# Kernel tuning notes

Measured on AMD Instinct MI355X. Metric: run time of the kernel, lower is better.

The kernel has to match this reference:

```python
import jax, jax.numpy as jnp
import numpy as np

N_NODES = 100000
N_FEAT = 512
HIDDEN = 64
N_CLASS = 40
N_EDGES = 3200000


def setup_inputs() -> dict:
    key = jax.random.key(0)
    k1, k2, k3, k4, k5, k6 = jax.random.split(key, 6)
    x = jax.random.normal(k1, (N_NODES, N_FEAT), dtype=jnp.float32)
    edge_index = jax.random.randint(k2, (2, N_EDGES), 0, N_NODES, dtype=jnp.int64)
    # Glorot-style init like PyG GCNConv
    s1 = (6.0 / (N_FEAT + HIDDEN)) ** 0.5
    s2 = (6.0 / (HIDDEN + N_CLASS)) ** 0.5
    W1 = jax.random.uniform(k3, (N_FEAT, HIDDEN), jnp.float32, -s1, s1)
    b1 = jnp.zeros((HIDDEN,), jnp.float32)
    W2 = jax.random.uniform(k4, (HIDDEN, N_CLASS), jnp.float32, -s2, s2)
    b2 = jnp.zeros((N_CLASS,), jnp.float32)
    return {"x": x, "edge_index": edge_index, "W1": W1, "b1": b1, "W2": W2, "b2": b2}


def _gcn_norm(edge_index, n_nodes):
    # add self-loops, symmetric normalization (PyG gcn_norm defaults)
    loops = jnp.arange(n_nodes, dtype=edge_index.dtype)
    src = jnp.concatenate([edge_index[0], loops])
    dst = jnp.concatenate([edge_index[1], loops])
    deg = jax.ops.segment_sum(jnp.ones_like(dst, dtype=jnp.float32), dst,
                              num_segments=n_nodes)
    dinv = jnp.where(deg > 0, jax.lax.rsqrt(deg), 0.0)
    norm = dinv[src] * dinv[dst]  # [E + N]
    return src, dst, norm


def _gcn_conv(h, src, dst, norm, W, b, n_nodes):
    h = h @ W                                   # [N, out]
    msg = h[src] * norm[:, None]                # gather + scale, [E+N, out]
    out = jax.ops.segment_sum(msg, dst, num_segments=n_nodes)  # scatter-add
    return out + b


def reference(x, edge_index, W1, b1, W2, b2):
    n = x.shape[0]
    src, dst, norm = _gcn_norm(edge_index, n)
    h = _gcn_conv(x, src, dst, norm, W1, b1, n)
    h = jax.nn.relu(h)
    h = _gcn_conv(h, src, dst, norm, W2, b2, n)
    return jax.nn.softmax(h, axis=-1)
```

## Files before the change

kernel.cpp:

```cpp
#include <hip/hip_runtime.h>
#include <hip/hip_bf16.h>
#include <math.h>

#define NFEAT 512
#define HID   64
#define NCLS  40
#define T2STRIDE 64

#define BSHIFT 9
#define BSIZE  512
#define BCAP   20480
#define CHUNK  4096

typedef __attribute__((ext_vector_type(8))) short bf16x8v;
typedef __attribute__((ext_vector_type(4))) float f32x4v;

__device__ __forceinline__ float rl_f(float v, int l) {
    return __int_as_float(__builtin_amdgcn_readlane(__float_as_int(v), l));
}
__device__ __forceinline__ unsigned short f2bf(float f) {
    __hip_bfloat16 h = __float2bfloat16(f);
    return *(unsigned short*)&h;
}


__global__ __launch_bounds__(256) void bin_scatter(const int* __restrict__ ei, int e,
                                                   int nbuckets,
                                                   int* __restrict__ bucket_cursor,
                                                   int* __restrict__ stage) {
    __shared__ int packed_s[CHUNK];
    __shared__ unsigned char bkt_s[CHUNK];
    __shared__ int hist[256];
    __shared__ int base_s[256];
    __shared__ int lcur[256];
    int t = threadIdx.x;
    int b0 = blockIdx.x * CHUNK;
    int cnt = min(CHUNK, e - b0);
    for (int i = t; i < 256; i += 256) hist[i] = 0;
    __syncthreads();
    for (int i = t; i < cnt; i += 256) {
        int s = ei[b0 + i];
        int d = ei[e + b0 + i];
        packed_s[i] = (s << BSHIFT) | (d & (BSIZE - 1));
        bkt_s[i] = (unsigned char)(d >> BSHIFT);
        atomicAdd(&hist[d >> BSHIFT], 1);
    }
    __syncthreads();
    for (int i = t; i < nbuckets; i += 256) {
        int c = hist[i];
        base_s[i] = c ? atomicAdd(&bucket_cursor[i], c) : 0;
        lcur[i] = 0;
    }
    __syncthreads();
    for (int i = t; i < cnt; i += 256) {
        int bk = bkt_s[i];
        int pos = base_s[bk] + atomicAdd(&lcur[bk], 1);
        if (pos < BCAP) stage[(size_t)bk * BCAP + pos] = packed_s[i];
    }
}

__global__ __launch_bounds__(256) void bucket_csr(const int* __restrict__ stage,
                                                  const int* __restrict__ bucket_cursor,
                                                  int* __restrict__ row_ptr,
                                                  float* __restrict__ dinv,
                                                  int* __restrict__ col,
                                                  int n, int e, int nbuckets) {
    __shared__ int sc[256];
    __shared__ int hist[BSIZE];
    __shared__ int lbase[BSIZE];
    __shared__ int psum[256];
    int b = blockIdx.x;
    int t = threadIdx.x;
    int v = (t < nbuckets) ? bucket_cursor[t] : 0;
    sc[t] = v;
    __syncthreads();
    #pragma unroll
    for (int off = 1; off < 256; off <<= 1) {
        int u = (t >= off) ? sc[t - off] : 0;
        __syncthreads();
        sc[t] += u;
        __syncthreads();
    }
    int base0 = (b > 0) ? sc[b - 1] : 0;
    if (b == 0 && t == 0) row_ptr[n] = e;

    int cnt = min(bucket_cursor[b], BCAP);
    int node0 = b << BSHIFT;
    int nnodes = min(BSIZE, n - node0);
    const int* st = stage + (size_t)b * BCAP;
    for (int i = t; i < BSIZE; i += 256) hist[i] = 0;
    __syncthreads();
    for (int i = t; i < cnt; i += 256) atomicAdd(&hist[st[i] & (BSIZE - 1)], 1);
    __syncthreads();
    int h0 = hist[2 * t], h1 = hist[2 * t + 1];
    int pair = h0 + h1;
    psum[t] = pair;
    __syncthreads();
    #pragma unroll
    for (int off = 1; off < 256; off <<= 1) {
        int u = (t >= off) ? psum[t - off] : 0;
        __syncthreads();
        psum[t] += u;
        __syncthreads();
    }
    int ex = psum[t] - pair;
    lbase[2 * t] = ex;
    lbase[2 * t + 1] = ex + h0;
    __syncthreads();
    for (int i = t; i < nnodes; i += 256) {
        row_ptr[node0 + i] = base0 + lbase[i];
        dinv[node0 + i] = rsqrtf((float)(hist[i] + 1));
    }
    __syncthreads();
    for (int i = t; i < cnt; i += 256) {
        int p = st[i];
        int pos = atomicAdd(&lbase[p & (BSIZE - 1)], 1);
        col[base0 + pos] = ((unsigned)p) >> BSHIFT;
    }
}


__global__ __launch_bounds__(256) void w1_to_bf16t(const float* __restrict__ W1,
                                                   unsigned short* __restrict__ w1bt) {
    int idx = blockIdx.x * 256 + threadIdx.x;
    int c = idx >> 9, k = idx & 511;
    w1bt[idx] = f2bf(W1[k * HID + c]);
}


__global__ __launch_bounds__(256) void gemm1(const float* __restrict__ x,
                                             const unsigned short* __restrict__ w1bt,
                                             const float* __restrict__ dinv,
                                             __hip_bfloat16* __restrict__ t1, int n) {
    __shared__ __align__(16) unsigned short As[64][40];
    __shared__ __align__(16) unsigned short Bs[64][40];
    int t = threadIdx.x;
    int m0 = blockIdx.x * 64;
    int w = t >> 6, lane = t & 63;
    int lrow = lane & 15, lkg = lane >> 4;
    f32x4v acc[4] = {};

    int arow = t >> 2;
    int akg = t & 3;
    int grow = m0 + arow; if (grow >= n) grow = n - 1;
    const float* xrow = x + (size_t)grow * NFEAT;

    for (int k0 = 0; k0 < NFEAT; k0 += 32) {
        float4 v0 = *(const float4*)(xrow + k0 + akg * 8);
        float4 v1 = *(const float4*)(xrow + k0 + akg * 8 + 4);
        union { unsigned short u[8]; uint4 q; } P;
        P.u[0] = f2bf(v0.x); P.u[1] = f2bf(v0.y); P.u[2] = f2bf(v0.z); P.u[3] = f2bf(v0.w);
        P.u[4] = f2bf(v1.x); P.u[5] = f2bf(v1.y); P.u[6] = f2bf(v1.z); P.u[7] = f2bf(v1.w);
        *(uint4*)&As[arow][akg * 8] = P.q;
        *(uint4*)&Bs[arow][akg * 8] = *(const uint4*)(w1bt + arow * 512 + k0 + akg * 8);
        __syncthreads();
        bf16x8v af = *(const bf16x8v*)&As[w * 16 + lrow][lkg * 8];
        #pragma unroll
        for (int nb = 0; nb < 4; nb++) {
            bf16x8v bfv = *(const bf16x8v*)&Bs[nb * 16 + lrow][lkg * 8];
            acc[nb] = __builtin_amdgcn_mfma_f32_16x16x32_bf16(af, bfv, acc[nb], 0, 0, 0);
        }
        __syncthreads();
    }
    #pragma unroll
    for (int r = 0; r < 4; r++) {
        int row = m0 + w * 16 + lkg * 4 + r;
        if (row < n) {
            float d = dinv[row];
            #pragma unroll
            for (int nb = 0; nb < 4; nb++) {
                t1[(size_t)row * HID + nb * 16 + lrow] = __float2bfloat16(acc[nb][r] * d);
            }
        }
    }
}


#define UNPACK_ADD(pv) do { \
    acc[0] += __uint_as_float((pv).x << 16); acc[1] += __uint_as_float((pv).x & 0xffff0000u); \
    acc[2] += __uint_as_float((pv).y << 16); acc[3] += __uint_as_float((pv).y & 0xffff0000u); \
    acc[4] += __uint_as_float((pv).z << 16); acc[5] += __uint_as_float((pv).z & 0xffff0000u); \
    acc[6] += __uint_as_float((pv).w << 16); acc[7] += __uint_as_float((pv).w & 0xffff0000u); } while (0)

__global__ __launch_bounds__(256) void agg1_gemm2(const __hip_bfloat16* __restrict__ t1,
                                                  const int* __restrict__ row_ptr,
                                                  const int* __restrict__ col,
                                                  const float* __restrict__ dinv,
                                                  const float* __restrict__ b1,
                                                  const float* __restrict__ W2,
                                                  __hip_bfloat16* __restrict__ t2, int n) {
    __shared__ float2 w2p[32 * 40];
    for (int i = threadIdx.x; i < 32 * 40; i += 256) {
        int k2 = i / 40, c = i - k2 * 40;
        w2p[i] = make_float2(W2[(2 * k2) * 40 + c], W2[(2 * k2 + 1) * 40 + c]);
    }
    __syncthreads();

    int wave = threadIdx.x >> 6;
    int lane = threadIdx.x & 63;
    int node0 = blockIdx.x * 4 + wave;
    int node = (node0 < n) ? node0 : n - 1;
    int r = lane & 7;
    int slot = lane >> 3;

    const uint4* t1q = (const uint4*)t1;
    int s0 = row_ptr[node], s1 = row_ptr[node + 1];

    float acc[8] = {0.f, 0.f, 0.f, 0.f, 0.f, 0.f, 0.f, 0.f};

    if (lane < 8) {
        uint4 pv = t1q[(size_t)node * 8 + lane];
        UNPACK_ADD(pv);
    }

    int bpbase = slot * 4;
    for (int jb = s0; jb < s1; jb += 32) {
        int rem = s1 - jb;
        int ll = lane & 31;
        int cidx = col[jb + ((ll < rem) ? ll : 0)];
        int srcg[4];
        #pragma unroll
        for (int g = 0; g < 4; g++) {
            int src = __builtin_amdgcn_ds_bpermute(bpbase + 32 * g, cidx);
            srcg[g] = (8 * g + slot < rem) ? src : n;
        }
        uint4 pv[4];
        #pragma unroll
        for (int g = 0; g < 4; g++) pv[g] = t1q[(size_t)srcg[g] * 8 + r];
        #pragma unroll
        for (int g = 0; g < 4; g++) { UNPACK_ADD(pv[g]); }
    }

    #pragma unroll
    for (int off = 8; off < 64; off <<= 1) {
        #pragma unroll
        for (int j = 0; j < 8; j++) acc[j] += __shfl_xor(acc[j], off, 64);
    }

    float dn = dinv[node];
    const float4* b1q = (const float4*)b1;
    float4 ba = b1q[2 * r];
    float4 bb = b1q[2 * r + 1];
    float hv[8];
    hv[0] = fmaxf(0.f, dn * acc[0] + ba.x);
    hv[1] = fmaxf(0.f, dn * acc[1] + ba.y);
    hv[2] = fmaxf(0.f, dn * acc[2] + ba.z);
    hv[3] = fmaxf(0.f, dn * acc[3] + ba.w);
    hv[4] = fmaxf(0.f, dn * acc[4] + bb.x);
    hv[5] = fmaxf(0.f, dn * acc[5] + bb.y);
    hv[6] = fmaxf(0.f, dn * acc[6] + bb.z);
    hv[7] = fmaxf(0.f, dn * acc[7] + bb.w);

    int c = (lane < 40) ? lane : 39;
    float o = 0.0f;
    #pragma unroll
    for (int rr = 0; rr < 8; rr++) {
        #pragma unroll
        for (int j2 = 0; j2 < 4; j2++) {
            float ha = rl_f(hv[2 * j2],     rr);
            float hb = rl_f(hv[2 * j2 + 1], rr);
            float2 wv = w2p[(4 * rr + j2) * 40 + c];
            o += ha * wv.x + hb * wv.y;
        }
    }
    if (node0 < n && lane < 40)
        t2[(size_t)node * T2STRIDE + lane] = __float2bfloat16(dn * o);
}


__global__ __launch_bounds__(256) void agg2_softmax(const __hip_bfloat16* __restrict__ t2,
                                                    const int* __restrict__ row_ptr,
                                                    const int* __restrict__ col,
                                                    const float* __restrict__ dinv,
                                                    const float* __restrict__ b2,
                                                    float* __restrict__ out, int n) {
    int wave = threadIdx.x >> 6;
    int lane = threadIdx.x & 63;
    int node = blockIdx.x * 4 + wave;
    if (node >= n) return;
    int h = lane >> 5;
    int p = lane & 31;
    int pc = (p < 20) ? p : 19;
    const unsigned* t2d = (const unsigned*)t2;
    int s0 = row_ptr[node], s1 = row_ptr[node + 1];

    float ax = 0.f, ay = 0.f;
    if (h == 0) {
        unsigned v = t2d[(size_t)node * 32 + pc];
        ax = __uint_as_float(v << 16);
        ay = __uint_as_float(v & 0xffff0000u);
    }
    for (int jb = s0; jb < s1; jb += 16) {
        int rem = s1 - jb;
        int cv = col[jb + ((lane < rem) ? lane : 0)];
        int srcg[8];
        #pragma unroll
        for (int i = 0; i < 8; i++) {
            int eid = 2 * i + h;
            int src = __builtin_amdgcn_ds_bpermute(4 * eid, cv);
            srcg[i] = (eid < rem) ? src : n;
        }
        unsigned pv[8];
        #pragma unroll
        for (int i = 0; i < 8; i++) pv[i] = t2d[(size_t)srcg[i] * 32 + pc];
        #pragma unroll
        for (int i = 0; i < 8; i++) {
            ax += __uint_as_float(pv[i] << 16);
            ay += __uint_as_float(pv[i] & 0xffff0000u);
        }
    }
    ax += __shfl_xor(ax, 32, 64);
    ay += __shfl_xor(ay, 32, 64);

    float dn = dinv[node];
    float2 bv = *(const float2*)(b2 + 2 * pc);
    float lx = dn * ax + bv.x;
    float ly = dn * ay + bv.y;
    float m = (p < 20) ? fmaxf(lx, ly) : -INFINITY;
    #pragma unroll
    for (int off = 16; off; off >>= 1) m = fmaxf(m, __shfl_xor(m, off, 64));
    float ex = (p < 20) ? expf(lx - m) : 0.0f;
    float ey = (p < 20) ? expf(ly - m) : 0.0f;
    float ssum = ex + ey;
    #pragma unroll
    for (int off = 16; off; off >>= 1) ssum += __shfl_xor(ssum, off, 64);
    if (h == 0 && p < 20) {
        *(float2*)(out + (size_t)node * NCLS + 2 * p) = make_float2(ex / ssum, ey / ssum);
    }
}


static inline size_t align256(size_t x) { return (x + 255) & ~(size_t)255; }

extern "C" void kernel_launch(void* const* d_in, const int* in_sizes, int n_in,
                              void* d_out, int out_size, void* d_ws, size_t ws_size,
                              hipStream_t stream) {
    const float* x  = (const float*)d_in[0];
    const int*   ei = (const int*)d_in[1];
    const float* W1 = (const float*)d_in[2];
    const float* b1 = (const float*)d_in[3];
    const float* W2 = (const float*)d_in[4];
    const float* b2 = (const float*)d_in[5];
    float* out = (float*)d_out;

    const int n = in_sizes[0] / NFEAT;
    const int e = in_sizes[1] / 2;
    const int nbuckets = (n + BSIZE - 1) >> BSHIFT;

    char* ws = (char*)d_ws;
    size_t off = 0;
    int*   row_ptr  = (int*)(ws + off);   off += align256((size_t)(n + 1) * 4);
    float* dinv     = (float*)(ws + off); off += align256((size_t)n * 4);
    int*   bcursor  = (int*)(ws + off);   off += align256(256 * 4);
    int*   col      = (int*)(ws + off);   off += align256((size_t)e * 4);
    int*   stage    = (int*)(ws + off);   off += align256((size_t)nbuckets * BCAP * 4);
    unsigned short* w1bt = (unsigned short*)(ws + off); off += align256((size_t)HID * NFEAT * 2);
    __hip_bfloat16* t1 = (__hip_bfloat16*)(ws + off); off += align256((size_t)(n + 1) * HID * 2);
    __hip_bfloat16* t2 = (__hip_bfloat16*)(ws + off); off += align256((size_t)(n + 1) * T2STRIDE * 2);

    (void)hipMemsetAsync(bcursor, 0, 256 * 4, stream);
    (void)hipMemsetAsync(t1 + (size_t)n * HID, 0, HID * 2, stream);
    (void)hipMemsetAsync(t2 + (size_t)n * T2STRIDE, 0, T2STRIDE * 2, stream);
    w1_to_bf16t<<<(HID * NFEAT) / 256, 256, 0, stream>>>(W1, w1bt);
    bin_scatter<<<(e + CHUNK - 1) / CHUNK, 256, 0, stream>>>(ei, e, nbuckets, bcursor, stage);
    bucket_csr<<<nbuckets, 256, 0, stream>>>(stage, bcursor, row_ptr, dinv, col, n, e, nbuckets);
    gemm1<<<(n + 63) / 64, 256, 0, stream>>>(x, w1bt, dinv, t1, n);
    agg1_gemm2<<<(n + 3) / 4, 256, 0, stream>>>(t1, row_ptr, col, dinv, b1, W2, t2, n);
    agg2_softmax<<<(n + 3) / 4, 256, 0, stream>>>(t2, row_ptr, col, dinv, b2, out, n);
}
```

Baseline: 550.8 us.

## Chunk features into 16-column slabs and reorder layer-2 aggregate before GEMM

Stores t1 and the hidden activations as four column-chunked slabs (32 bytes per node) so each aggregation block gathers from a smaller, more cache-resident table. A generic agg_pass kernel is launched twice. Each launch has blocks interleaved across chunks and halves of the node range, and each wave handles several nodes. Layer 2 now aggregates the 64-wide hidden features first and applies W2 afterwards in finish2, which adds fp32 intermediate round trips, extra launches, and 64- instead of 40-wide gathers for the second layer.

```diff
diff --git a/kernel.cpp b/kernel.cpp
--- a/kernel.cpp
+++ b/kernel.cpp
@@ -5,7 +5,7 @@
 #define NFEAT 512
 #define HID   64
 #define NCLS  40
-#define T2STRIDE 64
+#define NPW   4
 
 #define BSHIFT 9
 #define BSIZE  512
@@ -121,17 +121,21 @@
 
 
 __global__ __launch_bounds__(256) void w1_to_bf16t(const float* __restrict__ W1,
-                                                   unsigned short* __restrict__ w1bt) {
+                                                   unsigned short* __restrict__ w1bt,
+                                                   unsigned short* __restrict__ t1c, int n) {
     int idx = blockIdx.x * 256 + threadIdx.x;
     int c = idx >> 9, k = idx & 511;
     w1bt[idx] = f2bf(W1[k * HID + c]);
+    if (blockIdx.x == 0 && threadIdx.x < 32) {
+        ((unsigned*)t1c)[((size_t)(threadIdx.x >> 3) * (n + 1) + n) * 8 + (threadIdx.x & 7)] = 0;
+    }
 }
 
 
 __global__ __launch_bounds__(256) void gemm1(const float* __restrict__ x,
                                              const unsigned short* __restrict__ w1bt,
                                              const float* __restrict__ dinv,
-                                             __hip_bfloat16* __restrict__ t1, int n) {
+                                             unsigned short* __restrict__ t1c, int n) {
     __shared__ __align__(16) unsigned short As[64][40];
     __shared__ __align__(16) unsigned short Bs[64][40];
     int t = threadIdx.x;
@@ -169,164 +173,131 @@
             float d = dinv[row];
             #pragma unroll
             for (int nb = 0; nb < 4; nb++) {
-                t1[(size_t)row * HID + nb * 16 + lrow] = __float2bfloat16(acc[nb][r] * d);
+                t1c[((size_t)nb * (n + 1) + row) * 16 + lrow] =
+                    f2bf(acc[nb][r] * d);
             }
         }
     }
 }
 
 
-#define UNPACK_ADD(pv) do { \
-    acc[0] += __uint_as_float((pv).x << 16); acc[1] += __uint_as_float((pv).x & 0xffff0000u); \
-    acc[2] += __uint_as_float((pv).y << 16); acc[3] += __uint_as_float((pv).y & 0xffff0000u); \
-    acc[4] += __uint_as_float((pv).z << 16); acc[5] += __uint_as_float((pv).z & 0xffff0000u); \
-    acc[6] += __uint_as_float((pv).w << 16); acc[7] += __uint_as_float((pv).w & 0xffff0000u); } while (0)
-
-__global__ __launch_bounds__(256) void agg1_gemm2(const __hip_bfloat16* __restrict__ t1,
-                                                  const int* __restrict__ row_ptr,
-                                                  const int* __restrict__ col,
-                                                  const float* __restrict__ dinv,
-                                                  const float* __restrict__ b1,
-                                                  const float* __restrict__ W2,
-                                                  __hip_bfloat16* __restrict__ t2, int n) {
+__global__ __launch_bounds__(256) void agg_pass(const unsigned short* __restrict__ tc,
+                                                const int* __restrict__ row_ptr,
+                                                const int* __restrict__ col,
+                                                float* __restrict__ aggOut,
+                                                int n, int nsplit) {
+    int bid = blockIdx.x;
+    int x = bid & 7;
+    int chunk = x >> 1;
+    int half = x & 1;
+    int g = bid >> 3;
+    int wave = threadIdx.x >> 6;
+    int lane = threadIdx.x & 63;
+    int f = lane & 7;
+    int slot = lane >> 3;
+    const unsigned* tcu = (const unsigned*)tc + (size_t)chunk * (n + 1) * 8;
+    int nodebase = g * (4 * NPW) + wave * NPW + half * nsplit;
+    int nend = half ? n : nsplit;
+
+    for (int ni = 0; ni < NPW; ni++) {
+        int node = nodebase + ni;
+        if (node >= nend) break;
+        int s0 = row_ptr[node], s1 = row_ptr[node + 1];
+        float a0 = 0.f, a1 = 0.f;
+        if (slot == 0) {
+            unsigned v = tcu[node * 8 + f];
+            a0 = __uint_as_float(v << 16);
+            a1 = __uint_as_float(v & 0xffff0000u);
+        }
+        for (int jb = s0; jb < s1; jb += 64) {
+            int rem = s1 - jb;
+            int cv = col[jb + ((lane < rem) ? lane : 0)];
+            int src[8];
+            #pragma unroll
+            for (int i = 0; i < 8; i++) {
+                int eid = 8 * i + slot;
+                int sv = __builtin_amdgcn_ds_bpermute(4 * eid, cv);
+                src[i] = (eid < rem) ? sv : n;
+            }
+            unsigned pv[8];
+            #pragma unroll
+            for (int i = 0; i < 8; i++) pv[i] = tcu[src[i] * 8 + f];
+            #pragma unroll
+            for (int i = 0; i < 8; i++) {
+                a0 += __uint_as_float(pv[i] << 16);
+                a1 += __uint_as_float(pv[i] & 0xffff0000u);
+            }
+        }
+        #pragma unroll
+        for (int off = 8; off < 64; off <<= 1) {
+            a0 += __shfl_xor(a0, off, 64);
+            a1 += __shfl_xor(a1, off, 64);
+        }
+        if (slot == 0) {
+            *(float2*)(aggOut + (size_t)node * HID + chunk * 16 + 2 * f) =
+                make_float2(a0, a1);
+        }
+    }
+}
+
+
+__global__ __launch_bounds__(256) void finish1(const float* __restrict__ aggA,
+                                               const float* __restrict__ dinv,
+                                               const float* __restrict__ b1,
+                                               unsigned short* __restrict__ gc, int n) {
+    int t = threadIdx.x;
+    unsigned* gcu = (unsigned*)gc;
+    if (blockIdx.x == 0 && t < 32) {
+        gcu[((size_t)(t >> 3) * (n + 1) + n) * 8 + (t & 7)] = 0;
+    }
+    int idx = blockIdx.x * 256 + t;
+    int node = idx >> 5;
+    int fp = idx & 31;
+    if (node >= n) return;
+    float2 a = *(const float2*)(aggA + (size_t)node * HID + 2 * fp);
+    float dn = dinv[node];
+    float2 bv = *(const float2*)(b1 + 2 * fp);
+    float g0 = dn * fmaxf(0.f, dn * a.x + bv.x);
+    float g1 = dn * fmaxf(0.f, dn * a.y + bv.y);
+    unsigned p = ((unsigned)f2bf(g1) << 16) | (unsigned)f2bf(g0);
+    gcu[((size_t)(fp >> 3) * (n + 1) + node) * 8 + (fp & 7)] = p;
+}
+
+
+__global__ __launch_bounds__(256) void finish2(const float* __restrict__ aggB,
+                                               const float* __restrict__ dinv,
+                                               const float* __restrict__ W2,
+                                               const float* __restrict__ b2,
+                                               float* __restrict__ out, int n) {
     __shared__ float2 w2p[32 * 40];
     for (int i = threadIdx.x; i < 32 * 40; i += 256) {
         int k2 = i / 40, c = i - k2 * 40;
-        w2p[i] = make_float2(W2[(2 * k2) * 40 + c], W2[(2 * k2 + 1) * 40 + c]);
-    }
-    __syncthreads();
-
-    int wave = threadIdx.x >> 6;
-    int lane = threadIdx.x & 63;
-    int node0 = blockIdx.x * 4 + wave;
-    int node = (node0 < n) ? node0 : n - 1;
-    int r = lane & 7;
-    int slot = lane >> 3;
-
-    const uint4* t1q = (const uint4*)t1;
-    int s0 = row_ptr[node], s1 = row_ptr[node + 1];
-
-    float acc[8] = {0.f, 0.f, 0.f, 0.f, 0.f, 0.f, 0.f, 0.f};
-
-    if (lane < 8) {
-        uint4 pv = t1q[(size_t)node * 8 + lane];
-        UNPACK_ADD(pv);
-    }
-
-    int bpbase = slot * 4;
-    for (int jb = s0; jb < s1; jb += 32) {
-        int rem = s1 - jb;
-        int ll = lane & 31;
-        int cidx = col[jb + ((ll < rem) ? ll : 0)];
-        int srcg[4];
-        #pragma unroll
-        for (int g = 0; g < 4; g++) {
-            int src = __builtin_amdgcn_ds_bpermute(bpbase + 32 * g, cidx);
-            srcg[g] = (8 * g + slot < rem) ? src : n;
-        }
-        uint4 pv[4];
-        #pragma unroll
-        for (int g = 0; g < 4; g++) pv[g] = t1q[(size_t)srcg[g] * 8 + r];
-        #pragma unroll
-        for (int g = 0; g < 4; g++) { UNPACK_ADD(pv[g]); }
-    }
-
-    #pragma unroll
-    for (int off = 8; off < 64; off <<= 1) {
-        #pragma unroll
-        for (int j = 0; j < 8; j++) acc[j] += __shfl_xor(acc[j], off, 64);
-    }
-
-    float dn = dinv[node];
-    const float4* b1q = (const float4*)b1;
-    float4 ba = b1q[2 * r];
-    float4 bb = b1q[2 * r + 1];
-    float hv[8];
-    hv[0] = fmaxf(0.f, dn * acc[0] + ba.x);
-    hv[1] = fmaxf(0.f, dn * acc[1] + ba.y);
-    hv[2] = fmaxf(0.f, dn * acc[2] + ba.z);
-    hv[3] = fmaxf(0.f, dn * acc[3] + ba.w);
-    hv[4] = fmaxf(0.f, dn * acc[4] + bb.x);
-    hv[5] = fmaxf(0.f, dn * acc[5] + bb.y);
-    hv[6] = fmaxf(0.f, dn * acc[6] + bb.z);
-    hv[7] = fmaxf(0.f, dn * acc[7] + bb.w);
-
-    int c = (lane < 40) ? lane : 39;
-    float o = 0.0f;
-    #pragma unroll
-    for (int rr = 0; rr < 8; rr++) {
-        #pragma unroll
-        for (int j2 = 0; j2 < 4; j2++) {
-            float ha = rl_f(hv[2 * j2],     rr);
-            float hb = rl_f(hv[2 * j2 + 1], rr);
-            float2 wv = w2p[(4 * rr + j2) * 40 + c];
-            o += ha * wv.x + hb * wv.y;
-        }
-    }
-    if (node0 < n && lane < 40)
-        t2[(size_t)node * T2STRIDE + lane] = __float2bfloat16(dn * o);
-}
-
-
-__global__ __launch_bounds__(256) void agg2_softmax(const __hip_bfloat16* __restrict__ t2,
-                                                    const int* __restrict__ row_ptr,
-                                                    const int* __restrict__ col,
-                                                    const float* __restrict__ dinv,
-                                                    const float* __restrict__ b2,
-                                                    float* __restrict__ out, int n) {
-    int wave = threadIdx.x >> 6;
-    int lane = threadIdx.x & 63;
+        w2p[i] = make_float2(W2[(2 * k2) * NCLS + c], W2[(2 * k2 + 1) * NCLS + c]);
+    }
+    __syncthreads();
+    int wave = threadIdx.x >> 6, lane = threadIdx.x & 63;
     int node = blockIdx.x * 4 + wave;
     if (node >= n) return;
-    int h = lane >> 5;
-    int p = lane & 31;
-    int pc = (p < 20) ? p : 19;
-    const unsigned* t2d = (const unsigned*)t2;
-    int s0 = row_ptr[node], s1 = row_ptr[node + 1];
-
-    float ax = 0.f, ay = 0.f;
-    if (h == 0) {
-        unsigned v = t2d[(size_t)node * 32 + pc];
-        ax = __uint_as_float(v << 16);
-        ay = __uint_as_float(v & 0xffff0000u);
-    }
-    for (int jb = s0; jb < s1; jb += 16) {
-        int rem = s1 - jb;
-        int cv = col[jb + ((lane < rem) ? lane : 0)];
-        int srcg[8];
-        #pragma unroll
-        for (int i = 0; i < 8; i++) {
-            int eid = 2 * i + h;
-            int src = __builtin_amdgcn_ds_bpermute(4 * eid, cv);
-            srcg[i] = (eid < rem) ? src : n;
-        }
-        unsigned pv[8];
-        #pragma unroll
-        for (int i = 0; i < 8; i++) pv[i] = t2d[(size_t)srcg[i] * 32 + pc];
-        #pragma unroll
-        for (int i = 0; i < 8; i++) {
-            ax += __uint_as_float(pv[i] << 16);
-            ay += __uint_as_float(pv[i] & 0xffff0000u);
-        }
-    }
-    ax += __shfl_xor(ax, 32, 64);
-    ay += __shfl_xor(ay, 32, 64);
-
-    float dn = dinv[node];
-    float2 bv = *(const float2*)(b2 + 2 * pc);
-    float lx = dn * ax + bv.x;
-    float ly = dn * ay + bv.y;
-    float m = (p < 20) ? fmaxf(lx, ly) : -INFINITY;
-    #pragma unroll
-    for (int off = 16; off; off >>= 1) m = fmaxf(m, __shfl_xor(m, off, 64));
-    float ex = (p < 20) ? expf(lx - m) : 0.0f;
-    float ey = (p < 20) ? expf(ly - m) : 0.0f;
-    float ssum = ex + ey;
-    #pragma unroll
-    for (int off = 16; off; off >>= 1) ssum += __shfl_xor(ssum, off, 64);
-    if (h == 0 && p < 20) {
-        *(float2*)(out + (size_t)node * NCLS + 2 * p) = make_float2(ex / ssum, ey / ssum);
-    }
+    int q = lane & 31;
+    float2 hv = *(const float2*)(aggB + (size_t)node * HID + 2 * q);
+    int c = (lane < 40) ? lane : 39;
+    float o = 0.f;
+    #pragma unroll
+    for (int k = 0; k < 32; k++) {
+        float sx = rl_f(hv.x, k);
+        float sy = rl_f(hv.y, k);
+        float2 wv = w2p[k * 40 + c];
+        o += sx * wv.x + sy * wv.y;
+    }
+    float logit = dinv[node] * o + b2[c];
+    float m = (lane < 40) ? logit : -INFINITY;
+    #pragma unroll
+    for (int off = 32; off; off >>= 1) m = fmaxf(m, __shfl_xor(m, off, 64));
+    float ev = (lane < 40) ? expf(logit - m) : 0.0f;
+    float ssum = ev;
+    #pragma unroll
+    for (int off = 32; off; off >>= 1) ssum += __shfl_xor(ssum, off, 64);
+    if (lane < 40) out[(size_t)node * NCLS + lane] = ev / ssum;
 }
 
 
@@ -355,16 +326,21 @@
     int*   col      = (int*)(ws + off);   off += align256((size_t)e * 4);
     int*   stage    = (int*)(ws + off);   off += align256((size_t)nbuckets * BCAP * 4);
     unsigned short* w1bt = (unsigned short*)(ws + off); off += align256((size_t)HID * NFEAT * 2);
-    __hip_bfloat16* t1 = (__hip_bfloat16*)(ws + off); off += align256((size_t)(n + 1) * HID * 2);
-    __hip_bfloat16* t2 = (__hip_bfloat16*)(ws + off); off += align256((size_t)(n + 1) * T2STRIDE * 2);
+    unsigned short* t1c  = (unsigned short*)(ws + off); off += align256((size_t)4 * (n + 1) * 16 * 2);
+    unsigned short* gc   = (unsigned short*)(ws + off); off += align256((size_t)4 * (n + 1) * 16 * 2);
+    float* aggA = (float*)(ws + off);     off += align256((size_t)n * HID * 4);
+
+    const int nsplit = ((n + 7) / 8) * 4;
+    const int ghalf  = (nsplit + 4 * NPW - 1) / (4 * NPW);
+    const int aggblocks = ghalf * 8;
 
     (void)hipMemsetAsync(bcursor, 0, 256 * 4, stream);
-    (void)hipMemsetAsync(t1 + (size_t)n * HID, 0, HID * 2, stream);
-    (void)hipMemsetAsync(t2 + (size_t)n * T2STRIDE, 0, T2STRIDE * 2, stream);
-    w1_to_bf16t<<<(HID * NFEAT) / 256, 256, 0, stream>>>(W1, w1bt);
+    w1_to_bf16t<<<(HID * NFEAT) / 256, 256, 0, stream>>>(W1, w1bt, t1c, n);
     bin_scatter<<<(e + CHUNK - 1) / CHUNK, 256, 0, stream>>>(ei, e, nbuckets, bcursor, stage);
     bucket_csr<<<nbuckets, 256, 0, stream>>>(stage, bcursor, row_ptr, dinv, col, n, e, nbuckets);
-    gemm1<<<(n + 63) / 64, 256, 0, stream>>>(x, w1bt, dinv, t1, n);
-    agg1_gemm2<<<(n + 3) / 4, 256, 0, stream>>>(t1, row_ptr, col, dinv, b1, W2, t2, n);
-    agg2_softmax<<<(n + 3) / 4, 256, 0, stream>>>(t2, row_ptr, col, dinv, b2, out, n);
-}
+    gemm1<<<(n + 63) / 64, 256, 0, stream>>>(x, w1bt, dinv, t1c, n);
+    agg_pass<<<aggblocks, 256, 0, stream>>>(t1c, row_ptr, col, aggA, n, nsplit);
+    finish1<<<(n + 7) / 8, 256, 0, stream>>>(aggA, dinv, b1, gc, n);
+    agg_pass<<<aggblocks, 256, 0, stream>>>(gc, row_ptr, col, aggA, n, nsplit);
+    finish2<<<(n + 3) / 4, 256, 0, stream>>>(aggA, dinv, W2, b2, out, n);
+}
```

Result: slower. 639.5 us (+16.1%).

## Replace bucketed CSR build with global-atomic degree count, scan, and fill

Applied to the files above, without the earlier changes.

Swaps the two-pass bucket staging CSR construction for a counting-sort approach. It counts degrees with global atomics, takes a two-level prefix sum into row_ptr and cursor, then scatters source indices into col using per-node atomic cursors. It also switches several streaming loads (x rows, col indices) to nontemporal loads. The change removes the large staging buffer and the per-bucket capacity limit. In exchange it adds 3.2M scattered global atomics twice plus random col writes, and neighbor order within each row becomes nondeterministic.

```diff
diff --git a/kernel.cpp b/kernel.cpp
--- a/kernel.cpp
+++ b/kernel.cpp
@@ -7,13 +7,10 @@
 #define NCLS  40
 #define T2STRIDE 64
 
-#define BSHIFT 9
-#define BSIZE  512
-#define BCAP   20480
-#define CHUNK  4096
-
 typedef __attribute__((ext_vector_type(8))) short bf16x8v;
 typedef __attribute__((ext_vector_type(4))) float f32x4v;
+typedef __attribute__((ext_vector_type(4))) int   v4i;
+typedef __attribute__((ext_vector_type(4))) float v4f;
 
 __device__ __forceinline__ float rl_f(float v, int l) {
     return __int_as_float(__builtin_amdgcn_readlane(__float_as_int(v), l));
@@ -24,55 +21,56 @@
 }
 
 
-__global__ __launch_bounds__(256) void bin_scatter(const int* __restrict__ ei, int e,
-                                                   int nbuckets,
-                                                   int* __restrict__ bucket_cursor,
-                                                   int* __restrict__ stage) {
-    __shared__ int packed_s[CHUNK];
-    __shared__ unsigned char bkt_s[CHUNK];
-    __shared__ int hist[256];
-    __shared__ int base_s[256];
-    __shared__ int lcur[256];
-    int t = threadIdx.x;
-    int b0 = blockIdx.x * CHUNK;
-    int cnt = min(CHUNK, e - b0);
-    for (int i = t; i < 256; i += 256) hist[i] = 0;
+__global__ __launch_bounds__(256) void deg_count(const int* __restrict__ ei, int e,
+                                                 int* __restrict__ deg) {
+    int i4 = (blockIdx.x * 256 + threadIdx.x) * 4;
+    if (i4 + 3 < e) {
+        v4i d = __builtin_nontemporal_load((const v4i*)(ei + e + i4));
+        atomicAdd(&deg[d.x], 1);
+        atomicAdd(&deg[d.y], 1);
+        atomicAdd(&deg[d.z], 1);
+        atomicAdd(&deg[d.w], 1);
+    } else {
+        for (int i = i4; i < e; i++) atomicAdd(&deg[ei[e + i]], 1);
+    }
+}
+
+__global__ __launch_bounds__(256) void deg_bsum(const int* __restrict__ deg, int n,
+                                                int* __restrict__ bsum) {
+    __shared__ int red[256];
+    int idx = blockIdx.x * 256 + threadIdx.x;
+    red[threadIdx.x] = (idx < n) ? deg[idx] : 0;
     __syncthreads();
-    for (int i = t; i < cnt; i += 256) {
-        int s = ei[b0 + i];
-        int d = ei[e + b0 + i];
-        packed_s[i] = (s << BSHIFT) | (d & (BSIZE - 1));
-        bkt_s[i] = (unsigned char)(d >> BSHIFT);
-        atomicAdd(&hist[d >> BSHIFT], 1);
-    }
+    #pragma unroll
+    for (int off = 128; off; off >>= 1) {
+        if (threadIdx.x < off) red[threadIdx.x] += red[threadIdx.x + off];
+        __syncthreads();
+    }
+    if (threadIdx.x == 0) bsum[blockIdx.x] = red[0];
+}
+
+__global__ __launch_bounds__(256) void scan_emit(const int* __restrict__ deg,
+                                                 const int* __restrict__ bsum,
+                                                 int n, int e,
+                                                 int* __restrict__ row_ptr,
+                                                 int* __restrict__ cursor,
+                                                 float* __restrict__ dinv) {
+    __shared__ int partial[256];
+    __shared__ int sc[256];
+    int b = blockIdx.x, t = threadIdx.x;
+    int p = 0;
+    for (int i = t; i < b; i += 256) p += bsum[i];
+    partial[t] = p;
     __syncthreads();
-    for (int i = t; i < nbuckets; i += 256) {
-        int c = hist[i];
-        base_s[i] = c ? atomicAdd(&bucket_cursor[i], c) : 0;
-        lcur[i] = 0;
-    }
-    __syncthreads();
-    for (int i = t; i < cnt; i += 256) {
-        int bk = bkt_s[i];
-        int pos = base_s[bk] + atomicAdd(&lcur[bk], 1);
-        if (pos < BCAP) stage[(size_t)bk * BCAP + pos] = packed_s[i];
-    }
-}
-
-__global__ __launch_bounds__(256) void bucket_csr(const int* __restrict__ stage,
-                                                  const int* __restrict__ bucket_cursor,
-                                                  int* __restrict__ row_ptr,
-                                                  float* __restrict__ dinv,
-                                                  int* __restrict__ col,
-                                                  int n, int e, int nbuckets) {
-    __shared__ int sc[256];
-    __shared__ int hist[BSIZE];
-    __shared__ int lbase[BSIZE];
-    __shared__ int psum[256];
-    int b = blockIdx.x;
-    int t = threadIdx.x;
-    int v = (t < nbuckets) ? bucket_cursor[t] : 0;
-    sc[t] = v;
+    #pragma unroll
+    for (int off = 128; off; off >>= 1) {
+        if (t < off) partial[t] += partial[t + off];
+        __syncthreads();
+    }
+    int base = partial[0];
+    int idx = b * 256 + t;
+    int d = (idx < n) ? deg[idx] : 0;
+    sc[t] = d;
     __syncthreads();
     #pragma unroll
     for (int off = 1; off < 256; off <<= 1) {
@@ -81,41 +79,31 @@
         sc[t] += u;
         __syncthreads();
     }
-    int base0 = (b > 0) ? sc[b - 1] : 0;
+    if (idx < n) {
+        int rp = base + sc[t] - d;
+        row_ptr[idx] = rp;
+        cursor[idx] = rp;
+        dinv[idx] = rsqrtf((float)(d + 1));
+    }
     if (b == 0 && t == 0) row_ptr[n] = e;
-
-    int cnt = min(bucket_cursor[b], BCAP);
-    int node0 = b << BSHIFT;
-    int nnodes = min(BSIZE, n - node0);
-    const int* st = stage + (size_t)b * BCAP;
-    for (int i = t; i < BSIZE; i += 256) hist[i] = 0;
-    __syncthreads();
-    for (int i = t; i < cnt; i += 256) atomicAdd(&hist[st[i] & (BSIZE - 1)], 1);
-    __syncthreads();
-    int h0 = hist[2 * t], h1 = hist[2 * t + 1];
-    int pair = h0 + h1;
-    psum[t] = pair;
-    __syncthreads();
-    #pragma unroll
-    for (int off = 1; off < 256; off <<= 1) {
-        int u = (t >= off) ? psum[t - off] : 0;
-        __syncthreads();
-        psum[t] += u;
-        __syncthreads();
-    }
-    int ex = psum[t] - pair;
-    lbase[2 * t] = ex;
-    lbase[2 * t + 1] = ex + h0;
-    __syncthreads();
-    for (int i = t; i < nnodes; i += 256) {
-        row_ptr[node0 + i] = base0 + lbase[i];
-        dinv[node0 + i] = rsqrtf((float)(hist[i] + 1));
-    }
-    __syncthreads();
-    for (int i = t; i < cnt; i += 256) {
-        int p = st[i];
-        int pos = atomicAdd(&lbase[p & (BSIZE - 1)], 1);
-        col[base0 + pos] = ((unsigned)p) >> BSHIFT;
+}
+
+__global__ __launch_bounds__(256) void fill_col(const int* __restrict__ ei, int e,
+                                                int* __restrict__ cursor,
+                                                int* __restrict__ col) {
+    int i4 = (blockIdx.x * 256 + threadIdx.x) * 4;
+    if (i4 + 3 < e) {
+        v4i s = __builtin_nontemporal_load((const v4i*)(ei + i4));
+        v4i d = __builtin_nontemporal_load((const v4i*)(ei + e + i4));
+        int p0 = atomicAdd(&cursor[d.x], 1); col[p0] = s.x;
+        int p1 = atomicAdd(&cursor[d.y], 1); col[p1] = s.y;
+        int p2 = atomicAdd(&cursor[d.z], 1); col[p2] = s.z;
+        int p3 = atomicAdd(&cursor[d.w], 1); col[p3] = s.w;
+    } else {
+        for (int i = i4; i < e; i++) {
+            int p = atomicAdd(&cursor[ei[e + i]], 1);
+            col[p] = ei[i];
+        }
     }
 }
 
@@ -146,8 +134,8 @@
     const float* xrow = x + (size_t)grow * NFEAT;
 
     for (int k0 = 0; k0 < NFEAT; k0 += 32) {
-        float4 v0 = *(const float4*)(xrow + k0 + akg * 8);
-        float4 v1 = *(const float4*)(xrow + k0 + akg * 8 + 4);
+        v4f v0 = __builtin_nontemporal_load((const v4f*)(xrow + k0 + akg * 8));
+        v4f v1 = __builtin_nontemporal_load((const v4f*)(xrow + k0 + akg * 8 + 4));
         union { unsigned short u[8]; uint4 q; } P;
         P.u[0] = f2bf(v0.x); P.u[1] = f2bf(v0.y); P.u[2] = f2bf(v0.z); P.u[3] = f2bf(v0.w);
         P.u[4] = f2bf(v1.x); P.u[5] = f2bf(v1.y); P.u[6] = f2bf(v1.z); P.u[7] = f2bf(v1.w);
@@ -217,7 +205,7 @@
     for (int jb = s0; jb < s1; jb += 32) {
         int rem = s1 - jb;
         int ll = lane & 31;
-        int cidx = col[jb + ((ll < rem) ? ll : 0)];
+        int cidx = __builtin_nontemporal_load(col + jb + ((ll < rem) ? ll : 0));
         int srcg[4];
         #pragma unroll
         for (int g = 0; g < 4; g++) {
@@ -292,7 +280,7 @@
     }
     for (int jb = s0; jb < s1; jb += 16) {
         int rem = s1 - jb;
-        int cv = col[jb + ((lane < rem) ? lane : 0)];
+        int cv = __builtin_nontemporal_load(col + jb + ((lane < rem) ? lane : 0));
         int srcg[8];
         #pragma unroll
         for (int i = 0; i < 8; i++) {
@@ -345,25 +333,30 @@
 
     const int n = in_sizes[0] / NFEAT;
     const int e = in_sizes[1] / 2;
-    const int nbuckets = (n + BSIZE - 1) >> BSHIFT;
 
     char* ws = (char*)d_ws;
     size_t off = 0;
     int*   row_ptr  = (int*)(ws + off);   off += align256((size_t)(n + 1) * 4);
     float* dinv     = (float*)(ws + off); off += align256((size_t)n * 4);
-    int*   bcursor  = (int*)(ws + off);   off += align256(256 * 4);
+    int*   deg      = (int*)(ws + off);   off += align256((size_t)n * 4);
+    int*   cursor   = (int*)(ws + off);   off += align256((size_t)n * 4);
+    int*   bsum     = (int*)(ws + off);   off += align256(512 * 4);
     int*   col      = (int*)(ws + off);   off += align256((size_t)e * 4);
-    int*   stage    = (int*)(ws + off);   off += align256((size_t)nbuckets * BCAP * 4);
     unsigned short* w1bt = (unsigned short*)(ws + off); off += align256((size_t)HID * NFEAT * 2);
     __hip_bfloat16* t1 = (__hip_bfloat16*)(ws + off); off += align256((size_t)(n + 1) * HID * 2);
     __hip_bfloat16* t2 = (__hip_bfloat16*)(ws + off); off += align256((size_t)(n + 1) * T2STRIDE * 2);
 
-    (void)hipMemsetAsync(bcursor, 0, 256 * 4, stream);
+    const int nb256 = (n + 255) / 256;
+    const int eb4   = (e / 4 + 255) / 256;
+
+    (void)hipMemsetAsync(deg, 0, (size_t)n * 4, stream);
     (void)hipMemsetAsync(t1 + (size_t)n * HID, 0, HID * 2, stream);
     (void)hipMemsetAsync(t2 + (size_t)n * T2STRIDE, 0, T2STRIDE * 2, stream);
     w1_to_bf16t<<<(HID * NFEAT) / 256, 256, 0, stream>>>(W1, w1bt);
-    bin_scatter<<<(e + CHUNK - 1) / CHUNK, 256, 0, stream>>>(ei, e, nbuckets, bcursor, stage);
-    bucket_csr<<<nbuckets, 256, 0, stream>>>(stage, bcursor, row_ptr, dinv, col, n, e, nbuckets);
+    deg_count<<<eb4, 256, 0, stream>>>(ei, e, deg);
+    deg_bsum<<<nb256, 256, 0, stream>>>(deg, n, bsum);
+    scan_emit<<<nb256, 256, 0, stream>>>(deg, bsum, n, e, row_ptr, cursor, dinv);
+    fill_col<<<eb4, 256, 0, stream>>>(ei, e, cursor, col);
     gemm1<<<(n + 63) / 64, 256, 0, stream>>>(x, w1bt, dinv, t1, n);
     agg1_gemm2<<<(n + 3) / 4, 256, 0, stream>>>(t1, row_ptr, col, dinv, b1, W2, t2, n);
     agg2_softmax<<<(n + 3) / 4, 256, 0, stream>>>(t2, row_ptr, col, dinv, b2, out, n);
```

After: 884.6 us. +60.6%, slower.
